# Kernel optimization log

Hardware: AMD Instinct MI355X
Metric: run time of the kernel (lower is better)

Reference implementation:

```python
import jax, jax.numpy as jnp
import numpy as np

DIM_IN = 768
DIM_OUT = 64
SEQ = 4096
BATCH = 4

def setup_inputs() -> dict:
    key = jax.random.key(0)
    ks = jax.random.split(key, 7)
    s = 1.0 / np.sqrt(DIM_IN)
    return {
        "x": jax.random.normal(ks[0], (BATCH, SEQ, DIM_IN), dtype=jnp.float32),
        "wq": jax.random.uniform(ks[1], (DIM_IN, DIM_OUT), jnp.float32, -s, s),
        "bq": jax.random.uniform(ks[2], (DIM_OUT,), jnp.float32, -s, s),
        "wk": jax.random.uniform(ks[3], (DIM_IN, DIM_OUT), jnp.float32, -s, s),
        "bk": jax.random.uniform(ks[4], (DIM_OUT,), jnp.float32, -s, s),
        "wv": jax.random.uniform(ks[5], (DIM_IN, DIM_OUT), jnp.float32, -s, s),
        "bv": jax.random.uniform(ks[6], (DIM_OUT,), jnp.float32, -s, s),
    }

def reference(x, wq, bq, wk, bk, wv, bv):
    # QKV projections: (B, S, D_in) @ (D_in, D_out) + bias
    q = x @ wq + bq
    k = x @ wk + bk
    v = x @ wv + bv
    # full causal attention, scores scaled by sqrt(d_out) AFTER masking (as in source)
    scores = jnp.einsum('bqd,bkd->bqk', q, k)  # (B, S, S)
    seq = x.shape[1]
    causal = jnp.tril(jnp.ones((seq, seq), dtype=bool))  # True = keep
    scores = jnp.where(causal, scores, -jnp.inf)
    scale = 1.0 / np.sqrt(k.shape[-1]).astype(np.float32)
    weights = jax.nn.softmax(scores * scale, axis=-1)
    # dropout_rate = 0.0 -> identity
    return jnp.einsum('bqk,bkd->bqd', weights, v)
```

## Files before the change

kernel.cpp:

```cpp
#include <hip/hip_runtime.h>
#include <hip/hip_bf16.h>

#define BATCH 4
#define SEQ   4096
#define DIN   768
#define DOUT  64

typedef __attribute__((ext_vector_type(4))) float f32x4;
typedef __attribute__((ext_vector_type(8))) short short8;
typedef __attribute__((ext_vector_type(4))) short short4v;

#define QSCALE 0.18033688011112043f

static __device__ __forceinline__ unsigned short f2bf(float f) {
    union { float f; unsigned u; } un; un.f = f;
    unsigned r = un.u + 0x7FFF + ((un.u >> 16) & 1);
    return (unsigned short)(r >> 16);
}
static __device__ __forceinline__ float bf2f(unsigned short h) {
    union { unsigned u; float f; } un; un.u = ((unsigned)h) << 16;
    return un.f;
}

__global__ void wprep_kernel(const float* __restrict__ wq,
                             const float* __restrict__ wk,
                             const float* __restrict__ wv,
                             unsigned short* __restrict__ wF) {
    __shared__ float lds[64][65];
    int o = blockIdx.x / 12, kt = blockIdx.x % 12;
    const float* w = (o == 0) ? wq : (o == 1) ? wk : wv;
    int tid = threadIdx.x;
    int k0 = kt * 64;
    #pragma unroll
    for (int i = 0; i < 16; ++i) {
        int flat = tid + i * 256;
        int kl = flat >> 6, n = flat & 63;
        lds[kl][n] = w[(k0 + kl) * 64 + n];
    }
    __syncthreads();
    int lane = tid & 63;
    int m = lane & 15, g = lane >> 4;
    #pragma unroll
    for (int i = 0; i < 2; ++i) {
        int f = i * 4 + (tid >> 6);
        int t = f >> 1, kcl = f & 1;
        int kc = kt * 2 + kcl;
        int nc = o * 4 + t;
        short8 v;
        #pragma unroll
        for (int j = 0; j < 8; ++j)
            v[j] = (short)f2bf(lds[kcl * 32 + g * 8 + j][t * 16 + m]);
        *(short8*)&wF[(size_t)(nc * 24 + kc) * 512 + lane * 8] = v;
    }
}

__global__ void __launch_bounds__(256) proj_kernel(
        const float* __restrict__ x,
        const float* __restrict__ bq,
        const float* __restrict__ bk,
        const float* __restrict__ bv,
        const unsigned short* __restrict__ wF,
        unsigned short* __restrict__ Qf,
        unsigned short* __restrict__ Kf,
        unsigned short* __restrict__ Vf) {
    __shared__ __align__(16) unsigned short xs[32][776];
    __shared__ unsigned short tr[4][16][24];

    int tid = threadIdx.x;
    int w = tid >> 6;
    int lane = tid & 63;
    int m = lane & 15, g = lane >> 4;
    int r0 = blockIdx.x * 32;

    {
        const float* xbase = x + (size_t)r0 * DIN;
        #pragma unroll
        for (int i = 0; i < 24; ++i) {
            int flat4 = tid + i * 256;
            int row = flat4 / 192;
            int c4 = flat4 - row * 192;
            float4 v = *(const float4*)(xbase + (size_t)row * DIN + c4 * 4);
            short4v sv;
            sv[0] = (short)f2bf(v.x); sv[1] = (short)f2bf(v.y);
            sv[2] = (short)f2bf(v.z); sv[3] = (short)f2bf(v.w);
            *(short4v*)&xs[row][c4 * 4] = sv;
        }
    }
    __syncthreads();

    f32x4 acc[2][3];
    #pragma unroll
    for (int st = 0; st < 2; ++st)
        #pragma unroll
        for (int t = 0; t < 3; ++t) acc[st][t] = (f32x4){0.f, 0.f, 0.f, 0.f};

    for (int kc = 0; kc < 24; ++kc) {
        short8 af0 = *(const short8*)&xs[m][kc * 32 + g * 8];
        short8 af1 = *(const short8*)&xs[16 + m][kc * 32 + g * 8];
        #pragma unroll
        for (int tt = 0; tt < 3; ++tt) {
            int nc = w * 3 + tt;
            short8 bfrg = *(const short8*)(wF + (size_t)(nc * 24 + kc) * 512 + lane * 8);
            acc[0][tt] = __builtin_amdgcn_mfma_f32_16x16x32_bf16(af0, bfrg, acc[0][tt], 0, 0, 0);
            acc[1][tt] = __builtin_amdgcn_mfma_f32_16x16x32_bf16(af1, bfrg, acc[1][tt], 0, 0, 0);
        }
    }

    int b2 = r0 >> 12;
    int s = (r0 & 4095) >> 5;
    #pragma unroll
    for (int st = 0; st < 2; ++st) {
        #pragma unroll
        for (int tt = 0; tt < 3; ++tt) {
            int nc = w * 3 + tt;
            int o = nc >> 2;
            int t = nc & 3;
            const float* bias_p = (o == 0) ? bq : (o == 1) ? bk : bv;
            float bias = bias_p[t * 16 + m];
            #pragma unroll
            for (int r = 0; r < 4; ++r) {
                float val = acc[st][tt][r] + bias;
                if (o == 0) val *= QSCALE;
                tr[w][g * 4 + r][m] = f2bf(val);
            }
            if (o < 2) {
                if (g < 2) {
                    short8 v8;
                    #pragma unroll
                    for (int j = 0; j < 8; ++j) v8[j] = (short)tr[w][m][g * 8 + j];
                    unsigned short* dst = (o == 0) ? Qf : Kf;
                    int c = t >> 1;
                    *(short8*)&dst[(size_t)((blockIdx.x * 2 + st) * 2 + c) * 512
                                   + (((t & 1) * 2 + g) * 16 + m) * 8] = v8;
                }
            } else {
                if (g < 2) {
                    short8 v8;
                    #pragma unroll
                    for (int j = 0; j < 8; ++j) v8[j] = (short)tr[w][g * 8 + j][m];
                    *(short8*)&Vf[((size_t)(b2 * 128 + s) * 4 + t) * 512
                                  + ((st * 2 + g) * 16 + m) * 8] = v8;
                }
            }
        }
    }
}

__global__ void __launch_bounds__(512, 2) attn_kernel(
        const unsigned short* __restrict__ Qf,
        const unsigned short* __restrict__ Kf,
        const unsigned short* __restrict__ Vf,
        float* __restrict__ out) {
    __shared__ __align__(16) unsigned short P_lds[8][32][36];
    __shared__ __align__(16) unsigned short pacc[8][16][68];
    __shared__ float pm[8][16];
    __shared__ float pl[8][16];

    int j = blockIdx.x;
    int b = j & 3;
    int qt = j >> 2;
    int base0 = qt * 16;
    int base1 = (255 - qt) * 16;
    int ns0 = (qt + 2) >> 1;
    int ns1 = (257 - qt) >> 1;
    int tid = threadIdx.x;
    int w = tid >> 6;
    int lane = tid & 63;
    int m = lane & 15, g = lane >> 4;

    const unsigned short* Q0 = Qf + (size_t)(b * 256 + qt) * 1024 + lane * 8;
    const unsigned short* Q1 = Qf + (size_t)(b * 256 + 255 - qt) * 1024 + lane * 8;
    short8 qf[2][2];
    qf[0][0] = *(const short8*)(Q0);
    qf[0][1] = *(const short8*)(Q0 + 512);
    qf[1][0] = *(const short8*)(Q1);
    qf[1][1] = *(const short8*)(Q1 + 512);

    short8 onesB = (short8){0,0,0,0,0,0,0,0};
    if (m == 0) {
        #pragma unroll
        for (int jj = 0; jj < 8; ++jj) onesB[jj] = (short)0x3F80;
    }

    f32x4 acc[2][5];
    #pragma unroll
    for (int rt = 0; rt < 2; ++rt)
        #pragma unroll
        for (int t = 0; t < 5; ++t) acc[rt][t] = (f32x4){0.f, 0.f, 0.f, 0.f};
    float mrun[2][4];
    #pragma unroll
    for (int rt = 0; rt < 2; ++rt)
        #pragma unroll
        for (int r = 0; r < 4; ++r) mrun[rt][r] = -INFINITY;

    const unsigned short* Kbase = Kf + (size_t)(b * 256) * 1024 + lane * 8;
    const unsigned short* Vbase = Vf + (size_t)(b * 128) * 2048 + lane * 8;

    for (int s = w; s < ns1; s += 8) {
        int kv0 = s * 32;
        short8 kf[4];
        kf[0] = *(const short8*)(Kbase + (size_t)s * 2048);
        kf[1] = *(const short8*)(Kbase + (size_t)s * 2048 + 512);
        kf[2] = *(const short8*)(Kbase + (size_t)s * 2048 + 1024);
        kf[3] = *(const short8*)(Kbase + (size_t)s * 2048 + 1536);
        short8 vcur[4];
        #pragma unroll
        for (int t = 0; t < 4; ++t)
            vcur[t] = *(const short8*)(Vbase + (size_t)s * 2048 + t * 512);

        #pragma unroll
        for (int rt = 0; rt < 2; ++rt) {
            if (rt == 0 && s >= ns0) continue;
            int qbase = (rt == 0) ? base0 : base1;
            bool lastd = (s == ((rt == 0) ? ns0 : ns1) - 1);

            f32x4 sc[2];
            sc[0] = (f32x4){0.f, 0.f, 0.f, 0.f};
            sc[1] = (f32x4){0.f, 0.f, 0.f, 0.f};
            sc[0] = __builtin_amdgcn_mfma_f32_16x16x32_bf16(qf[rt][0], kf[0], sc[0], 0, 0, 0);
            sc[0] = __builtin_amdgcn_mfma_f32_16x16x32_bf16(qf[rt][1], kf[1], sc[0], 0, 0, 0);
            sc[1] = __builtin_amdgcn_mfma_f32_16x16x32_bf16(qf[rt][0], kf[2], sc[1], 0, 0, 0);
            sc[1] = __builtin_amdgcn_mfma_f32_16x16x32_bf16(qf[rt][1], kf[3], sc[1], 0, 0, 0);

            if (lastd) {
                #pragma unroll
                for (int tt = 0; tt < 2; ++tt)
                    #pragma unroll
                    for (int r = 0; r < 4; ++r)
                        if (kv0 + tt * 16 + m > qbase + g * 4 + r) sc[tt][r] = -INFINITY;
            }

            bool need = false;
            #pragma unroll
            for (int r = 0; r < 4; ++r) {
                float th = mrun[rt][r] + 8.0f;
                need = need | (sc[0][r] > th) | (sc[1][r] > th);
            }
            if (__any(need)) {
                float rmax[4];
                #pragma unroll
                for (int r = 0; r < 4; ++r) rmax[r] = fmaxf(sc[0][r], sc[1][r]);
                #pragma unroll
                for (int msk = 1; msk <= 8; msk <<= 1)
                    #pragma unroll
                    for (int r = 0; r < 4; ++r)
                        rmax[r] = fmaxf(rmax[r], __shfl_xor(rmax[r], msk));
                #pragma unroll
                for (int r = 0; r < 4; ++r) {
                    float mnew = fmaxf(mrun[rt][r], rmax[r]);
                    float alpha = __builtin_amdgcn_exp2f(mrun[rt][r] - mnew);
                    mrun[rt][r] = mnew;
                    #pragma unroll
                    for (int t = 0; t < 5; ++t) acc[rt][t][r] *= alpha;
                }
            }

            #pragma unroll
            for (int tt = 0; tt < 2; ++tt)
                #pragma unroll
                for (int r = 0; r < 4; ++r)
                    P_lds[w][rt * 16 + g * 4 + r][tt * 16 + m] =
                        f2bf(__builtin_amdgcn_exp2f(sc[tt][r] - mrun[rt][r]));
            short8 pa = *(const short8*)&P_lds[w][rt * 16 + m][g * 8];

            #pragma unroll
            for (int t = 0; t < 4; ++t)
                acc[rt][t] = __builtin_amdgcn_mfma_f32_16x16x32_bf16(pa, vcur[t], acc[rt][t], 0, 0, 0);
            acc[rt][4] = __builtin_amdgcn_mfma_f32_16x16x32_bf16(pa, onesB, acc[rt][4], 0, 0, 0);
        }
    }

    #pragma unroll
    for (int rt = 0; rt < 2; ++rt) {
        int qbase = (rt == 0) ? base0 : base1;
        if (m == 0) {
            #pragma unroll
            for (int r = 0; r < 4; ++r) {
                pm[w][g * 4 + r] = mrun[rt][r];
                pl[w][g * 4 + r] = acc[rt][4][r];
            }
        }
        #pragma unroll
        for (int t = 0; t < 4; ++t)
            #pragma unroll
            for (int r = 0; r < 4; ++r)
                pacc[w][g * 4 + r][t * 16 + m] = f2bf(acc[rt][t][r]);
        __syncthreads();

        if (tid < 256) {
            int row = tid >> 4;
            int c4 = (tid & 15) * 4;
            float mmax = pm[0][row];
            #pragma unroll
            for (int w2 = 1; w2 < 8; ++w2) mmax = fmaxf(mmax, pm[w2][row]);
            float lt = 0.f;
            float o0 = 0.f, o1 = 0.f, o2 = 0.f, o3 = 0.f;
            #pragma unroll
            for (int w2 = 0; w2 < 8; ++w2) {
                float sc2 = __builtin_amdgcn_exp2f(pm[w2][row] - mmax);
                lt += pl[w2][row] * sc2;
                short4v pa4 = *(const short4v*)&pacc[w2][row][c4];
                o0 += bf2f((unsigned short)pa4[0]) * sc2;
                o1 += bf2f((unsigned short)pa4[1]) * sc2;
                o2 += bf2f((unsigned short)pa4[2]) * sc2;
                o3 += bf2f((unsigned short)pa4[3]) * sc2;
            }
            float invl = 1.0f / lt;
            float4 res = make_float4(o0 * invl, o1 * invl, o2 * invl, o3 * invl);
            *(float4*)&out[(size_t)(b * SEQ + qbase + row) * DOUT + c4] = res;
        }
        __syncthreads();
    }
}

extern "C" void kernel_launch(void* const* d_in, const int* in_sizes, int n_in,
                              void* d_out, int out_size, void* d_ws, size_t ws_size,
                              hipStream_t stream) {
    const float* x  = (const float*)d_in[0];
    const float* wq = (const float*)d_in[1];
    const float* bq = (const float*)d_in[2];
    const float* wk = (const float*)d_in[3];
    const float* bk = (const float*)d_in[4];
    const float* wv = (const float*)d_in[5];
    const float* bv = (const float*)d_in[6];
    float* out = (float*)d_out;

    char* ws = (char*)d_ws;
    unsigned short* wF = (unsigned short*)ws;
    unsigned short* Qf = (unsigned short*)(ws + 294912);
    unsigned short* Kf = (unsigned short*)(ws + 294912 + 2097152);
    unsigned short* Vf = (unsigned short*)(ws + 294912 + 4194304);

    wprep_kernel<<<36, 256, 0, stream>>>(wq, wk, wv, wF);
    proj_kernel<<<512, 256, 0, stream>>>(x, bq, bk, bv, wF, Qf, Kf, Vf);
    attn_kernel<<<512, 512, 0, stream>>>(Qf, Kf, Vf, out);
}
```

Before: 53.33 us.

## Double-buffer K/V register loads and relax launch bounds to one block

Prefetches the next K and V fragments into registers while the current tile's QK and PV MFMAs run, hiding global load latency behind compute. Launch bounds are lowered from 2 to 1 block per CU so the compiler has room for the extra prefetch registers. This risks lower occupancy, with fewer waves available to hide latency across blocks.

Result: slower. 56.85 us (+6.6%).

```diff
diff --git a/kernel.cpp b/kernel.cpp
--- a/kernel.cpp
+++ b/kernel.cpp
@@ -146,7 +146,7 @@
     }
 }
 
-__global__ void __launch_bounds__(512, 2) attn_kernel(
+__global__ void __launch_bounds__(512, 1) attn_kernel(
         const unsigned short* __restrict__ Qf,
         const unsigned short* __restrict__ Kf,
         const unsigned short* __restrict__ Vf,
@@ -196,17 +196,26 @@
     const unsigned short* Kbase = Kf + (size_t)(b * 256) * 1024 + lane * 8;
     const unsigned short* Vbase = Vf + (size_t)(b * 128) * 2048 + lane * 8;
 
+    short8 kf[4], vf[4];
+    if (w < ns1) {
+        #pragma unroll
+        for (int t = 0; t < 4; ++t) {
+            kf[t] = *(const short8*)(Kbase + (size_t)w * 2048 + t * 512);
+            vf[t] = *(const short8*)(Vbase + (size_t)w * 2048 + t * 512);
+        }
+    }
+
     for (int s = w; s < ns1; s += 8) {
         int kv0 = s * 32;
-        short8 kf[4];
-        kf[0] = *(const short8*)(Kbase + (size_t)s * 2048);
-        kf[1] = *(const short8*)(Kbase + (size_t)s * 2048 + 512);
-        kf[2] = *(const short8*)(Kbase + (size_t)s * 2048 + 1024);
-        kf[3] = *(const short8*)(Kbase + (size_t)s * 2048 + 1536);
-        short8 vcur[4];
-        #pragma unroll
-        for (int t = 0; t < 4; ++t)
-            vcur[t] = *(const short8*)(Vbase + (size_t)s * 2048 + t * 512);
+        int sn = s + 8;
+        short8 kn[4], vn[4];
+        if (sn < ns1) {
+            #pragma unroll
+            for (int t = 0; t < 4; ++t) {
+                kn[t] = *(const short8*)(Kbase + (size_t)sn * 2048 + t * 512);
+                vn[t] = *(const short8*)(Vbase + (size_t)sn * 2048 + t * 512);
+            }
+        }
 
         #pragma unroll
         for (int rt = 0; rt < 2; ++rt) {
@@ -265,8 +274,13 @@
 
             #pragma unroll
             for (int t = 0; t < 4; ++t)
-                acc[rt][t] = __builtin_amdgcn_mfma_f32_16x16x32_bf16(pa, vcur[t], acc[rt][t], 0, 0, 0);
+                acc[rt][t] = __builtin_amdgcn_mfma_f32_16x16x32_bf16(pa, vf[t], acc[rt][t], 0, 0, 0);
             acc[rt][4] = __builtin_amdgcn_mfma_f32_16x16x32_bf16(pa, onesB, acc[rt][4], 0, 0, 0);
+        }
+
+        if (sn < ns1) {
+            #pragma unroll
+            for (int t = 0; t < 4; ++t) { kf[t] = kn[t]; vf[t] = vn[t]; }
         }
     }
 
```
